# Kernel tuning notes

Hardware: AMD Instinct MI355X
Metric: run time of the kernel (lower is better)

## Reference

```python
import jax, jax.numpy as jnp
import numpy as np

WINDOW = 16  # window_size from init_kwargs


def sigmoid_cutoff(x):
    # max(min(1.2*sigmoid(x) - 0.1, 1), 0)
    return jnp.clip(1.2 * jax.nn.sigmoid(x) - 0.1, 0.0, 1.0)


def setup_inputs() -> dict:
    key = jax.random.key(0)
    k1, k2, k3 = jax.random.split(key, 3)
    B, S, H = 8, 2048, 1024
    x = jax.random.normal(k1, (B, S, H), dtype=jnp.float32)
    # Dense kernels (glorot-ish scale), x_layer has no bias, y_layer has bias
    Wx = jax.random.normal(k2, (H, H), dtype=jnp.float32) * (1.0 / np.sqrt(H))
    Wy = jax.random.normal(k3, (H, 2 * H), dtype=jnp.float32) * (1.0 / np.sqrt(H))
    by = jnp.zeros((2 * H,), dtype=jnp.float32)
    return {"x": x, "Wx": Wx, "Wy": Wy, "by": by}


def reference(x, Wx, Wy, by):
    B, S, H = x.shape
    # left-pad sequence with window_size-1 zeros, then project once (x_layer)
    xp = jnp.pad(x, ((0, 0), (WINDOW - 1, 0), (0, 0)))
    proj = jnp.einsum('bsh,hd->bsd', xp, Wx)  # [B, S+W-1, H]

    def step(state, i):
        # inputs[:, i:S+i] in the original loop
        inp = jax.lax.dynamic_slice_in_dim(proj, i, S, axis=1)  # [B,S,H]
        ns = jnp.einsum('bsh,hd->bsd', state, Wy) + by          # [B,S,2H]
        # reshape [B,S,2,H]: channel 0 = candidate, channel 1 = gate
        cand, gate_logits = jnp.split(ns, 2, axis=-1)
        gate = sigmoid_cutoff(gate_logits)
        new_state = jax.nn.relu(gate * (inp + cand) + (1.0 - gate) * state)
        return new_state, None

    state0 = jnp.zeros_like(x)
    state, _ = jax.lax.scan(step, state0, jnp.arange(WINDOW))
    return state
```

## Files before the change

kernel.cpp:

```cpp
#include <hip/hip_runtime.h>

#define H 1024
#define SEQ 2048
#define MROWS 16384
#define KD 1024
#define NTK 16
#define EPW 72

typedef _Float16 f16;
typedef _Float16 f16x8 __attribute__((ext_vector_type(8)));
typedef float f32x4 __attribute__((ext_vector_type(4)));

__device__ __forceinline__ float gate_fn(float x) {
    float s = 1.0f / (1.0f + __expf(-x));
    return fminf(fmaxf(1.2f * s - 0.1f, 0.0f), 1.0f);
}

__device__ __forceinline__ void gload_lds16(const void* g, void* lds) {
    __builtin_amdgcn_global_load_lds(
        (const __attribute__((address_space(1))) unsigned int*)g,
        (__attribute__((address_space(3))) unsigned int*)lds, 16, 0, 0);
}

__global__ void k_f32_to_f16(const float* __restrict__ in, f16* __restrict__ out) {
    size_t i = ((size_t)blockIdx.x * blockDim.x + threadIdx.x) * 8;
    float4 v0 = *(const float4*)(in + i);
    float4 v1 = *(const float4*)(in + i + 4);
    f16x8 o;
    o[0] = (f16)v0.x; o[1] = (f16)v0.y; o[2] = (f16)v0.z; o[3] = (f16)v0.w;
    o[4] = (f16)v1.x; o[5] = (f16)v1.y; o[6] = (f16)v1.z; o[7] = (f16)v1.w;
    *(f16x8*)(out + i) = o;
}

__global__ void k_transpose_f16(const float* __restrict__ Wsrc, f16* __restrict__ WT,
                                int K, int N) {
    __shared__ float tile[32][33];
    int n0 = blockIdx.x * 32, k0 = blockIdx.y * 32;
    for (int i = threadIdx.y; i < 32; i += 8)
        tile[i][threadIdx.x] = Wsrc[(size_t)(k0 + i) * N + n0 + threadIdx.x];
    __syncthreads();
    for (int i = threadIdx.y; i < 32; i += 8)
        WT[(size_t)(n0 + i) * K + k0 + threadIdx.x] = (f16)tile[threadIdx.x][i];
}

__global__ __launch_bounds__(256) void k_proj_gemm(const f16* __restrict__ A,
                                                   const f16* __restrict__ BT,
                                                   f16* __restrict__ P16) {
    __shared__ alignas(16) f16 Alds[128 * 32];
    __shared__ alignas(16) f16 Blds[128 * 32];
    const int tid = threadIdx.x;
    const int lane = tid & 63, wid = tid >> 6;
    const int l15 = lane & 15, l4 = lane >> 4;
    const int bm = blockIdx.x, bn = blockIdx.y;

    const f16* gA[2]; const f16* gB[2];
    char* ldsA[2]; char* ldsB[2];
#pragma unroll
    for (int it = 0; it < 2; ++it) {
        int c = it * 4 + wid;
        int row = c * 16 + (lane >> 2);
        int kch = (lane & 3) ^ ((row >> 1) & 3);
        gA[it] = A + (size_t)(bm * 128 + row) * KD + kch * 8;
        gB[it] = BT + (size_t)(bn * 128 + row) * KD + kch * 8;
        ldsA[it] = (char*)Alds + c * 1024;
        ldsB[it] = (char*)Blds + c * 1024;
    }

    int offA[2], offB[8];
#pragma unroll
    for (int m = 0; m < 2; ++m) {
        int row = wid * 32 + m * 16 + l15;
        offA[m] = row * 64 + ((l4 ^ ((row >> 1) & 3)) << 4);
    }
#pragma unroll
    for (int n = 0; n < 8; ++n) {
        int row = n * 16 + l15;
        offB[n] = row * 64 + ((l4 ^ ((row >> 1) & 3)) << 4);
    }

    f32x4 acc[2][8] = {};

    for (int kt = 0; kt < KD / 32; ++kt) {
        __syncthreads();
#pragma unroll
        for (int it = 0; it < 2; ++it) {
            gload_lds16(gA[it], ldsA[it]);
            gload_lds16(gB[it], ldsB[it]);
            gA[it] += 32; gB[it] += 32;
        }
        __syncthreads();
        f16x8 a[2], b[8];
#pragma unroll
        for (int m = 0; m < 2; ++m) a[m] = *(const f16x8*)((const char*)Alds + offA[m]);
#pragma unroll
        for (int n = 0; n < 8; ++n) b[n] = *(const f16x8*)((const char*)Blds + offB[n]);
#pragma unroll
        for (int n = 0; n < 8; ++n)
#pragma unroll
            for (int m = 0; m < 2; ++m)
                acc[m][n] = __builtin_amdgcn_mfma_f32_16x16x32_f16(a[m], b[n], acc[m][n], 0, 0, 0);
    }

#pragma unroll
    for (int m = 0; m < 2; ++m)
#pragma unroll
        for (int n = 0; n < 8; ++n) {
            int col = bn * 128 + n * 16 + l15;
#pragma unroll
            for (int r = 0; r < 4; ++r) {
                int row = bm * 128 + wid * 32 + m * 16 + l4 * 4 + r;
                P16[(size_t)row * H + col] = (f16)acc[m][n][r];
            }
        }
}

__global__ void k_step0(const f16* __restrict__ P16, const float* __restrict__ by,
                        f16* __restrict__ S16) {
    size_t idx = ((size_t)blockIdx.x * blockDim.x + threadIdx.x) * 8;
    int row = (int)(idx >> 10);
    int d = (int)(idx & 1023);
    int s = row & (SEQ - 1);
    f16x8 p = {};
    if (s >= 15) p = *(const f16x8*)(P16 + (size_t)(row - 15) * H + d);
    float4 byc0 = *(const float4*)(by + d);
    float4 byc1 = *(const float4*)(by + d + 4);
    float4 byg0 = *(const float4*)(by + H + d);
    float4 byg1 = *(const float4*)(by + H + d + 4);
    f16x8 sv;
#pragma unroll
    for (int j = 0; j < 8; ++j) {
        float byc = (j < 4) ? ((const float*)&byc0)[j] : ((const float*)&byc1)[j - 4];
        float byg = (j < 4) ? ((const float*)&byg0)[j] : ((const float*)&byg1)[j - 4];
        float g = gate_fn(byg);
        float v = fmaxf(g * ((float)p[j] + byc), 0.f);
        sv[j] = (f16)v;
    }
    *(f16x8*)(S16 + idx) = sv;
}

__global__ __launch_bounds__(512) void k_step_gemm256(const f16* __restrict__ A,
                                                      const f16* __restrict__ BT,
                                                      const f16* __restrict__ P16,
                                                      const float* __restrict__ by,
                                                      float* __restrict__ Out,
                                                      f16* __restrict__ Snext,
                                                      int stepi) {
    __shared__ alignas(16) char lds[131072];
    const int tid = threadIdx.x;
    const int lane = tid & 63, w = tid >> 6;
    const int l15 = lane & 15, l4 = lane >> 4;
    const int wr = w >> 2, wc = w & 3;

    const int orig = blockIdx.x;
    const int wg = (orig & 7) * 64 + (orig >> 3);
    const int bm = wg >> 3, cbn = wg & 7;

    const int r0 = w * 16 + (lane >> 2), r1 = r0 + 128;
    const int slot = (lane & 3) ^ ((r0 >> 1) & 3);
    const char* pA0 = (const char*)A + ((size_t)(bm * 256 + r0) * KD + slot * 8) * 2;
    const char* pA1 = (const char*)A + ((size_t)(bm * 256 + r1) * KD + slot * 8) * 2;
    const int gB0 = ((r0 >> 5) & 1) * H + cbn * 128 + (r0 >> 6) * 32 + (r0 & 31);
    const int gB1 = ((r1 >> 5) & 1) * H + cbn * 128 + (r1 >> 6) * 32 + (r1 & 31);
    const char* pB0 = (const char*)BT + ((size_t)gB0 * KD + slot * 8) * 2;
    const char* pB1 = (const char*)BT + ((size_t)gB1 * KD + slot * 8) * 2;
    const int dst = w * 1024 + lane * 16;

#define STA(bp, kh) do { gload_lds16(pA0 + (kh)*64, (bp) + (kh)*16384 + dst); \
                         gload_lds16(pA1 + (kh)*64, (bp) + (kh)*16384 + 8192 + dst); } while (0)
#define STB(bp, kh) do { gload_lds16(pB0 + (kh)*64, (bp) + 32768 + (kh)*16384 + dst); \
                         gload_lds16(pB1 + (kh)*64, (bp) + 32768 + (kh)*16384 + 8192 + dst); } while (0)

    const int sx = (l4 ^ ((l15 >> 1) & 3)) << 4;
    int offA[8], offB[4];
#pragma unroll
    for (int m = 0; m < 8; ++m) offA[m] = (wr * 128 + m * 16 + l15) * 64 + sx;
#pragma unroll
    for (int n = 0; n < 4; ++n) offB[n] = 32768 + (wc * 64 + n * 16 + l15) * 64 + sx;

    f32x4 acc[8][4] = {};
    f16x8 av[4], bv[4];

    char* cb = lds;
    char* nx = lds + 65536;

    STA(cb, 0); STB(cb, 0); STA(cb, 1); STB(cb, 1);
    pA0 += 128; pA1 += 128; pB0 += 128; pB1 += 128;

    for (int t = 0; t < NTK; ++t) {
        const bool pf = (t + 1 < NTK);
        if (pf) STA(nx, 0);
        asm volatile("s_waitcnt vmcnt(4)" ::: "memory");
        __builtin_amdgcn_s_barrier();
        __builtin_amdgcn_sched_barrier(0);
#pragma unroll
        for (int m = 0; m < 4; ++m) av[m] = *(const f16x8*)(cb + offA[m]);
#pragma unroll
        for (int n = 0; n < 4; ++n) bv[n] = *(const f16x8*)(cb + offB[n]);
        __builtin_amdgcn_s_setprio(1);
#pragma unroll
        for (int m = 0; m < 4; ++m)
#pragma unroll
            for (int n = 0; n < 4; ++n)
                acc[m][n] = __builtin_amdgcn_mfma_f32_16x16x32_f16(av[m], bv[n], acc[m][n], 0, 0, 0);
        __builtin_amdgcn_s_setprio(0);
        __builtin_amdgcn_sched_barrier(0);
        if (pf) STB(nx, 0);
        __builtin_amdgcn_s_barrier();
        __builtin_amdgcn_sched_barrier(0);
#pragma unroll
        for (int m = 0; m < 4; ++m) av[m] = *(const f16x8*)(cb + offA[4 + m]);
        __builtin_amdgcn_s_setprio(1);
#pragma unroll
        for (int m = 0; m < 4; ++m)
#pragma unroll
            for (int n = 0; n < 4; ++n)
                acc[4 + m][n] = __builtin_amdgcn_mfma_f32_16x16x32_f16(av[m], bv[n], acc[4 + m][n], 0, 0, 0);
        __builtin_amdgcn_s_setprio(0);
        __builtin_amdgcn_sched_barrier(0);
        if (pf) STA(nx, 1);
        if (pf) { asm volatile("s_waitcnt vmcnt(4)" ::: "memory"); }
        else    { asm volatile("s_waitcnt vmcnt(0)" ::: "memory"); }
        __builtin_amdgcn_s_barrier();
        __builtin_amdgcn_sched_barrier(0);
#pragma unroll
        for (int m = 0; m < 4; ++m) av[m] = *(const f16x8*)(cb + 16384 + offA[m]);
#pragma unroll
        for (int n = 0; n < 4; ++n) bv[n] = *(const f16x8*)(cb + 16384 + offB[n]);
        __builtin_amdgcn_s_setprio(1);
#pragma unroll
        for (int m = 0; m < 4; ++m)
#pragma unroll
            for (int n = 0; n < 4; ++n)
                acc[m][n] = __builtin_amdgcn_mfma_f32_16x16x32_f16(av[m], bv[n], acc[m][n], 0, 0, 0);
        __builtin_amdgcn_s_setprio(0);
        __builtin_amdgcn_sched_barrier(0);
        if (pf) STB(nx, 1);
        __builtin_amdgcn_s_barrier();
        __builtin_amdgcn_sched_barrier(0);
#pragma unroll
        for (int m = 0; m < 4; ++m) av[m] = *(const f16x8*)(cb + 16384 + offA[4 + m]);
        __builtin_amdgcn_s_setprio(1);
#pragma unroll
        for (int m = 0; m < 4; ++m)
#pragma unroll
            for (int n = 0; n < 4; ++n)
                acc[4 + m][n] = __builtin_amdgcn_mfma_f32_16x16x32_f16(av[m], bv[n], acc[4 + m][n], 0, 0, 0);
        __builtin_amdgcn_s_setprio(0);
        __builtin_amdgcn_sched_barrier(0);
        if (pf) { pA0 += 128; pA1 += 128; pB0 += 128; pB1 += 128; }
        char* tmp = cb; cb = nx; nx = tmp;
    }
    asm volatile("s_waitcnt vmcnt(0)" ::: "memory");
    __syncthreads();
#undef STA
#undef STB

    const bool last = (stepi == 15);
    f16* Cand = (f16*)lds;
    f16* Gate = (f16*)(lds + 256 * EPW * 2);
#pragma unroll
    for (int rnd = 0; rnd < 2; ++rnd) {
#pragma unroll
        for (int m = 0; m < 8; ++m)
#pragma unroll
            for (int r4 = 0; r4 < 4; ++r4) {
                int row = wr * 128 + m * 16 + l4 * 4 + r4;
                int cr = wc * 16 + l15;
                Cand[row * EPW + cr] = (f16)acc[m][rnd][r4];
                Gate[row * EPW + cr] = (f16)acc[m][rnd + 2][r4];
            }
        __syncthreads();
        const int g = tid & 7;
        const int rb = tid >> 3;
        const int ctile = (g >> 1) * 32 + rnd * 16 + (g & 1) * 8;
        const int d = cbn * 128 + ctile;
        const int cr0 = g * 8;
        float4 byc0 = *(const float4*)(by + d);
        float4 byc1 = *(const float4*)(by + d + 4);
        float4 byg0 = *(const float4*)(by + H + d);
        float4 byg1 = *(const float4*)(by + H + d + 4);
#pragma unroll
        for (int p = 0; p < 4; ++p) {
            int row = p * 64 + rb;
            int grow = bm * 256 + row;
            int s = grow & (SEQ - 1);
            f16x8 c8 = *(const f16x8*)(Cand + row * EPW + cr0);
            f16x8 g8 = *(const f16x8*)(Gate + row * EPW + cr0);
            f16x8 p8 = {};
            if (s >= 15 - stepi)
                p8 = *(const f16x8*)(P16 + (size_t)(grow + stepi - 15) * H + d);
            f16x8 s8 = *(const f16x8*)(A + (size_t)grow * H + d);
            f16x8 o8; float ov[8];
#pragma unroll
            for (int j = 0; j < 8; ++j) {
                float byc = (j < 4) ? ((const float*)&byc0)[j] : ((const float*)&byc1)[j - 4];
                float byg = (j < 4) ? ((const float*)&byg0)[j] : ((const float*)&byg1)[j - 4];
                float cand = (float)c8[j] + byc;
                float gg = gate_fn((float)g8[j] + byg);
                float v = fmaxf(gg * ((float)p8[j] + cand) + (1.f - gg) * (float)s8[j], 0.f);
                o8[j] = (f16)v; ov[j] = v;
            }
            if (!last) {
                *(f16x8*)(Snext + (size_t)grow * H + d) = o8;
            } else {
                *(float4*)(Out + (size_t)grow * H + d) = make_float4(ov[0], ov[1], ov[2], ov[3]);
                *(float4*)(Out + (size_t)grow * H + d + 4) = make_float4(ov[4], ov[5], ov[6], ov[7]);
            }
        }
        __syncthreads();
    }
}

extern "C" void kernel_launch(void* const* d_in, const int* in_sizes, int n_in,
                              void* d_out, int out_size, void* d_ws, size_t ws_size,
                              hipStream_t stream) {
    (void)in_sizes; (void)n_in; (void)out_size; (void)ws_size;
    const float* x  = (const float*)d_in[0];
    const float* Wx = (const float*)d_in[1];
    const float* Wy = (const float*)d_in[2];
    const float* by = (const float*)d_in[3];
    float* out = (float*)d_out;

    char* ws = (char*)d_ws;
    const size_t MB = 1024ull * 1024ull;
    f16* st16a = (f16*)(ws);
    f16* st16b = (f16*)(ws + 32 * MB);
    f16* P16   = (f16*)(ws + 64 * MB);
    f16* WxT   = (f16*)(ws + 96 * MB);
    f16* WyT   = (f16*)(ws + 98 * MB);

    hipLaunchKernelGGL(k_f32_to_f16, dim3(MROWS * H / 8 / 256), dim3(256), 0, stream, x, st16a);
    hipLaunchKernelGGL(k_transpose_f16, dim3(H / 32, H / 32), dim3(32, 8), 0, stream, Wx, WxT, H, H);
    hipLaunchKernelGGL(k_transpose_f16, dim3(2 * H / 32, H / 32), dim3(32, 8), 0, stream, Wy, WyT, H, 2 * H);
    hipLaunchKernelGGL(k_proj_gemm, dim3(MROWS / 128, H / 128), dim3(256), 0, stream, st16a, WxT, P16);
    hipLaunchKernelGGL(k_step0, dim3(MROWS * H / 8 / 256), dim3(256), 0, stream, P16, by, st16b);

    f16* bufs[2] = {st16a, st16b};
    for (int i = 1; i <= 15; ++i) {
        const f16* cur = bufs[i & 1];
        f16* nxt = bufs[(i + 1) & 1];
        hipLaunchKernelGGL(k_step_gemm256, dim3(MROWS / 256 * 8), dim3(512), 0, stream,
                           cur, WyT, P16, by, out, nxt, i);
    }
}
```

Before: 1.329 ms.

## Double-buffer LDS-to-register fragments to overlap ds_reads with MFMA

Restructures the GEMM main loop so the A/B fragments for the next MFMA block are read from LDS into a second register set while the current block's MFMAs run. Global-to-LDS prefetches are regrouped as paired A+B issues, and the next tile's first fragments are loaded before the loop advances. This hides LDS read latency behind matrix math, at the cost of more VGPRs for the extra fragment registers, which could lower occupancy. It also changes where waits and barriers sit, so the synchronization ordering is less obviously safe.

```diff
diff --git a/kernel.cpp b/kernel.cpp
--- a/kernel.cpp
+++ b/kernel.cpp
@@ -178,73 +178,77 @@
     for (int n = 0; n < 4; ++n) offB[n] = 32768 + (wc * 64 + n * 16 + l15) * 64 + sx;
 
     f32x4 acc[8][4] = {};
-    f16x8 av[4], bv[4];
+    f16x8 AV0[4], AV1[4], BV0[4], BV1[4];
 
     char* cb = lds;
     char* nx = lds + 65536;
 
     STA(cb, 0); STB(cb, 0); STA(cb, 1); STB(cb, 1);
     pA0 += 128; pA1 += 128; pB0 += 128; pB1 += 128;
+    asm volatile("s_waitcnt vmcnt(0)" ::: "memory");
+    __syncthreads();
+#pragma unroll
+    for (int m = 0; m < 4; ++m) AV0[m] = *(const f16x8*)(cb + offA[m]);
+#pragma unroll
+    for (int n = 0; n < 4; ++n) BV0[n] = *(const f16x8*)(cb + offB[n]);
 
     for (int t = 0; t < NTK; ++t) {
         const bool pf = (t + 1 < NTK);
-        if (pf) STA(nx, 0);
-        asm volatile("s_waitcnt vmcnt(4)" ::: "memory");
-        __builtin_amdgcn_s_barrier();
-        __builtin_amdgcn_sched_barrier(0);
-#pragma unroll
-        for (int m = 0; m < 4; ++m) av[m] = *(const f16x8*)(cb + offA[m]);
-#pragma unroll
-        for (int n = 0; n < 4; ++n) bv[n] = *(const f16x8*)(cb + offB[n]);
-        __builtin_amdgcn_s_setprio(1);
-#pragma unroll
-        for (int m = 0; m < 4; ++m)
-#pragma unroll
-            for (int n = 0; n < 4; ++n)
-                acc[m][n] = __builtin_amdgcn_mfma_f32_16x16x32_f16(av[m], bv[n], acc[m][n], 0, 0, 0);
-        __builtin_amdgcn_s_setprio(0);
-        __builtin_amdgcn_sched_barrier(0);
-        if (pf) STB(nx, 0);
-        __builtin_amdgcn_s_barrier();
-        __builtin_amdgcn_sched_barrier(0);
-#pragma unroll
-        for (int m = 0; m < 4; ++m) av[m] = *(const f16x8*)(cb + offA[4 + m]);
-        __builtin_amdgcn_s_setprio(1);
-#pragma unroll
-        for (int m = 0; m < 4; ++m)
-#pragma unroll
-            for (int n = 0; n < 4; ++n)
-                acc[4 + m][n] = __builtin_amdgcn_mfma_f32_16x16x32_f16(av[m], bv[n], acc[4 + m][n], 0, 0, 0);
-        __builtin_amdgcn_s_setprio(0);
-        __builtin_amdgcn_sched_barrier(0);
-        if (pf) STA(nx, 1);
+#pragma unroll
+        for (int m = 0; m < 4; ++m) AV1[m] = *(const f16x8*)(cb + offA[4 + m]);
+        if (pf) { STA(nx, 0); STB(nx, 0); }
         if (pf) { asm volatile("s_waitcnt vmcnt(4)" ::: "memory"); }
         else    { asm volatile("s_waitcnt vmcnt(0)" ::: "memory"); }
         __builtin_amdgcn_s_barrier();
         __builtin_amdgcn_sched_barrier(0);
-#pragma unroll
-        for (int m = 0; m < 4; ++m) av[m] = *(const f16x8*)(cb + 16384 + offA[m]);
-#pragma unroll
-        for (int n = 0; n < 4; ++n) bv[n] = *(const f16x8*)(cb + 16384 + offB[n]);
         __builtin_amdgcn_s_setprio(1);
 #pragma unroll
         for (int m = 0; m < 4; ++m)
 #pragma unroll
             for (int n = 0; n < 4; ++n)
-                acc[m][n] = __builtin_amdgcn_mfma_f32_16x16x32_f16(av[m], bv[n], acc[m][n], 0, 0, 0);
+                acc[m][n] = __builtin_amdgcn_mfma_f32_16x16x32_f16(AV0[m], BV0[n], acc[m][n], 0, 0, 0);
         __builtin_amdgcn_s_setprio(0);
-        __builtin_amdgcn_sched_barrier(0);
-        if (pf) STB(nx, 1);
+#pragma unroll
+        for (int m = 0; m < 4; ++m) AV0[m] = *(const f16x8*)(cb + 16384 + offA[m]);
+#pragma unroll
+        for (int n = 0; n < 4; ++n) BV1[n] = *(const f16x8*)(cb + 16384 + offB[n]);
+        if (pf) { STA(nx, 1); STB(nx, 1); }
         __builtin_amdgcn_s_barrier();
         __builtin_amdgcn_sched_barrier(0);
-#pragma unroll
-        for (int m = 0; m < 4; ++m) av[m] = *(const f16x8*)(cb + 16384 + offA[4 + m]);
         __builtin_amdgcn_s_setprio(1);
 #pragma unroll
         for (int m = 0; m < 4; ++m)
 #pragma unroll
             for (int n = 0; n < 4; ++n)
-                acc[4 + m][n] = __builtin_amdgcn_mfma_f32_16x16x32_f16(av[m], bv[n], acc[4 + m][n], 0, 0, 0);
+                acc[4 + m][n] = __builtin_amdgcn_mfma_f32_16x16x32_f16(AV1[m], BV0[n], acc[4 + m][n], 0, 0, 0);
+        __builtin_amdgcn_s_setprio(0);
+#pragma unroll
+        for (int m = 0; m < 4; ++m) AV1[m] = *(const f16x8*)(cb + 16384 + offA[4 + m]);
+        if (pf) { asm volatile("s_waitcnt vmcnt(4)" ::: "memory"); }
+        else    { asm volatile("s_waitcnt vmcnt(0)" ::: "memory"); }
+        __builtin_amdgcn_s_barrier();
+        __builtin_amdgcn_sched_barrier(0);
+        __builtin_amdgcn_s_setprio(1);
+#pragma unroll
+        for (int m = 0; m < 4; ++m)
+#pragma unroll
+            for (int n = 0; n < 4; ++n)
+                acc[m][n] = __builtin_amdgcn_mfma_f32_16x16x32_f16(AV0[m], BV1[n], acc[m][n], 0, 0, 0);
+        __builtin_amdgcn_s_setprio(0);
+        if (pf) {
+#pragma unroll
+            for (int m = 0; m < 4; ++m) AV0[m] = *(const f16x8*)(nx + offA[m]);
+#pragma unroll
+            for (int n = 0; n < 4; ++n) BV0[n] = *(const f16x8*)(nx + offB[n]);
+        }
+        __builtin_amdgcn_s_barrier();
+        __builtin_amdgcn_sched_barrier(0);
+        __builtin_amdgcn_s_setprio(1);
+#pragma unroll
+        for (int m = 0; m < 4; ++m)
+#pragma unroll
+            for (int n = 0; n < 4; ++n)
+                acc[4 + m][n] = __builtin_amdgcn_mfma_f32_16x16x32_f16(AV1[m], BV1[n], acc[4 + m][n], 0, 0, 0);
         __builtin_amdgcn_s_setprio(0);
         __builtin_amdgcn_sched_barrier(0);
         if (pf) { pA0 += 128; pA1 += 128; pB0 += 128; pB1 += 128; }
```

New measurement: 1.362 ms. 1.02x slower.
